# Kernel optimization log

Measured on AMD Instinct MI355X. Metric: run time of the kernel, lower is better.

The kernel has to match this reference:

```python
import jax, jax.numpy as jnp
import numpy as np
from jax import lax

# Conv3d(in_dim, in_dim, kernel=(1,3,3), padding=(0,1,1)) == per-time-slice 3x3 conv mixing channels

def _conv3d(x, w, b):
    # x: [B, C, T, W, H], w: [O, I, 1, 3, 3], b: [O]
    y = lax.conv_general_dilated(
        x, w,
        window_strides=(1, 1, 1),
        padding=[(0, 0), (1, 1), (1, 1)],
        dimension_numbers=("NCDHW", "OIDHW", "NCDHW"),
    )
    return y + b[None, :, None, None, None]


def setup_inputs() -> dict:
    key = jax.random.key(0)
    ks = jax.random.split(key, 8)
    B, C, T, W, H = 8, 64, 16, 64, 64
    fan = C * 1 * 3 * 3
    bound = 1.0 / np.sqrt(fan)  # torch Conv3d default init range
    x = jax.random.normal(ks[0], (B, C, T, W, H), dtype=jnp.float32)
    wq = jax.random.uniform(ks[1], (C, C, 1, 3, 3), jnp.float32, -bound, bound)
    wk = jax.random.uniform(ks[2], (C, C, 1, 3, 3), jnp.float32, -bound, bound)
    wv = jax.random.uniform(ks[3], (C, C, 1, 3, 3), jnp.float32, -bound, bound)
    bq = jax.random.uniform(ks[4], (C,), jnp.float32, -bound, bound)
    bk = jax.random.uniform(ks[5], (C,), jnp.float32, -bound, bound)
    bv = jax.random.uniform(ks[6], (C,), jnp.float32, -bound, bound)
    # torch init is gamma=0 (identity output); use nonzero so reference exercises the full path
    gamma = jax.random.normal(ks[7], (1,), dtype=jnp.float32) * 0.1
    return {"x": x, "wq": wq, "wk": wk, "wv": wv,
            "bq": bq, "bk": bk, "bv": bv, "gamma": gamma}


def reference(x, wq, wk, wv, bq, bk, bv, gamma):
    B, C, T, W, H = x.shape
    WH = W * H
    q = _conv3d(x, wq, bq).reshape(B, C, T, WH)
    k = _conv3d(x, wk, bk).reshape(B, C, T, WH)
    v = _conv3d(x, wv, bv).reshape(B, C, T, WH)
    # Original: (q[...,:,None] @ k[...,None,:]) @ v[...,:,None]  -> rank-1 energy, no softmax.
    # Exact reassociation: out_i = q_i * sum_j(k_j * v_j), avoiding the [WH, WH] matrix.
    s = jnp.sum(k * v, axis=-1, keepdims=True)  # [B, C, T, 1]
    out = (q * s).reshape(B, C, T, W, H)
    return gamma[0] * out + x
```

## Files before the change

kernel.cpp:

```cpp
#include <hip/hip_runtime.h>
#include <hip/hip_bf16.h>
#include <stdint.h>

typedef __attribute__((ext_vector_type(8))) short bf16x8;
typedef __attribute__((ext_vector_type(4))) float f32x4v;
typedef __attribute__((ext_vector_type(16))) float f32x16;
typedef __attribute__((ext_vector_type(4))) unsigned int u32x4;

#define CH_STRIDE 65536

__device__ __forceinline__ uint16_t f2bf(float f) {
  uint32_t u = __builtin_bit_cast(uint32_t, f);
  u = (u + 0x7FFFu + ((u >> 16) & 1u)) >> 16;
  return (uint16_t)u;
}
__device__ __forceinline__ float bf2f(uint32_t b) {
  return __builtin_bit_cast(float, b << 16);
}
__device__ __forceinline__ uint16_t cvt_bf(float f) {
  return __builtin_bit_cast(uint16_t, __float2bfloat16(f));
}
__device__ __forceinline__ bf16x8 andm(bf16x8 v, uint32_t m) {
  u32x4 u = __builtin_bit_cast(u32x4, v);
  u[0] &= m; u[1] &= m; u[2] &= m; u[3] &= m;
  return __builtin_bit_cast(bf16x8, u);
}

#define MFMA32(a, b, c) __builtin_amdgcn_mfma_f32_32x32x16_bf16(a, b, c, 0, 0, 0)
#define WAIT0 asm volatile("s_waitcnt vmcnt(0) lgkmcnt(0)" ::: "memory")
#define BAR __builtin_amdgcn_s_barrier()
#define SCHED0 __builtin_amdgcn_sched_barrier(0)

#define LDSX6  (6 * 8 * 66 * 16)
#define LDSK   (6 * 8 * 64 * 16)

__device__ __forceinline__ void gld16(const void* g, void* l) {
  __builtin_amdgcn_global_load_lds(
      (const __attribute__((address_space(1))) uint32_t*)g,
      (__attribute__((address_space(3))) uint32_t*)l, 16, 0, 0);
}

__device__ __forceinline__ bf16x8 ldx(const uint8_t* ldsx, int row, int oct, int ci) {
  return *(const bf16x8*)(ldsx + (uint32_t)((row * 8 + oct) * 66 + ci) * 16u);
}
__device__ __forceinline__ bf16x8 ldx64(const uint8_t* ldsx, int row, int oct, int ci) {
  return *(const bf16x8*)(ldsx + (uint32_t)((row * 8 + oct) * 64 + ci) * 16u);
}
__device__ __forceinline__ bf16x8 ldw_kv(const uint8_t* ldsw, int oct, int rowloc) {
  return *(const bf16x8*)(ldsw + (uint32_t)(oct * 128 + rowloc) * 16u);
}
__device__ __forceinline__ bf16x8 ldw_q(const uint8_t* ldsw, int oct, int row) {
  return *(const bf16x8*)(ldsw + (uint32_t)(oct * 64 + row) * 16u);
}

__device__ __forceinline__ void stage_unit66(uint8_t* ldsx, const float* xs, int w0, int u) {
  int row = u >> 7, oct = (u >> 4) & 7, g = u & 15;
  int w = w0 - 1 + row;
  uint32_t base = (uint32_t)((row * 8 + oct) * 66 + 4 * g + 1) * 16u;
  if ((unsigned)w < 64u) {
    const float* p = xs + (size_t)(oct * 8) * CH_STRIDE + w * 64 + 4 * g;
    f32x4v v[8];
    #pragma unroll
    for (int j = 0; j < 8; ++j) v[j] = *(const f32x4v*)(p + (size_t)j * CH_STRIDE);
    #pragma unroll
    for (int c = 0; c < 4; ++c) {
      bf16x8 frag;
      #pragma unroll
      for (int q = 0; q < 4; ++q) {
        frag[2 * q]     = (short)cvt_bf(v[2 * q][c]);
        frag[2 * q + 1] = (short)cvt_bf(v[2 * q + 1][c]);
      }
      *(bf16x8*)(ldsx + base + (uint32_t)c * 16u) = frag;
    }
  } else {
    bf16x8 z = {};
    #pragma unroll
    for (int c = 0; c < 4; ++c) *(bf16x8*)(ldsx + base + (uint32_t)c * 16u) = z;
  }
}
__device__ __forceinline__ void stage_unit64(uint8_t* ldsx, const float* xs, int w0, int u) {
  int row = u >> 7, oct = (u >> 4) & 7, g = u & 15;
  int w = w0 - 1 + row;
  uint32_t base = (uint32_t)((row * 8 + oct) * 64 + 4 * g) * 16u;
  if ((unsigned)w < 64u) {
    const float* p = xs + (size_t)(oct * 8) * CH_STRIDE + w * 64 + 4 * g;
    f32x4v v[8];
    #pragma unroll
    for (int j = 0; j < 8; ++j) v[j] = *(const f32x4v*)(p + (size_t)j * CH_STRIDE);
    #pragma unroll
    for (int c = 0; c < 4; ++c) {
      bf16x8 frag;
      #pragma unroll
      for (int q = 0; q < 4; ++q) {
        frag[2 * q]     = (short)cvt_bf(v[2 * q][c]);
        frag[2 * q + 1] = (short)cvt_bf(v[2 * q + 1][c]);
      }
      *(bf16x8*)(ldsx + base + (uint32_t)c * 16u) = frag;
    }
  } else {
    bf16x8 z = {};
    #pragma unroll
    for (int c = 0; c < 4; ++c) *(bf16x8*)(ldsx + base + (uint32_t)c * 16u) = z;
  }
}
__device__ __forceinline__ void stage_halo66(uint8_t* ldsx, int tid, int nrow) {
  if (tid < nrow * 16) {
    int row = tid >> 4, rem = tid & 15;
    int oct = rem >> 1, side = rem & 1;
    bf16x8 z = {};
    *(bf16x8*)(ldsx + (uint32_t)((row * 8 + oct) * 66 + side * 65) * 16u) = z;
  }
}

__global__ void prep_weights(const float* __restrict__ wq, const float* __restrict__ wk,
                             const float* __restrict__ wv, uint16_t* __restrict__ wout) {
  int i = blockIdx.x * 256 + threadIdx.x;
  if (i >= 110592) return;
  if (i < 36864) {
    int tap = i >> 12, oct = (i >> 9) & 7, row = (i >> 3) & 63, j = i & 7;
    wout[i] = f2bf(wq[(row * 64 + oct * 8 + j) * 9 + tap]);
  } else {
    int m = i - 36864;
    int tap = m >> 13, oct = (m >> 10) & 7, rl = (m >> 3) & 127, j = m & 7;
    const float* src = (rl < 64) ? wk : wv;
    wout[i] = f2bf(src[((rl & 63) * 64 + oct * 8 + j) * 9 + tap]);
  }
}

__global__ __launch_bounds__(256, 2) void kv_s_kernel(
    const float* __restrict__ x, const uint16_t* __restrict__ wkv,
    const float* __restrict__ bk, const float* __restrict__ bv,
    float* __restrict__ s_out) {
  extern __shared__ uint8_t lds[];
  uint8_t* ldsx = lds;
  uint8_t* ldswA = lds + LDSK;
  uint8_t* ldswB = lds + LDSK + 16384;
  const int tid = threadIdx.x;
  const int l = tid & 63;
  const int ng = tid >> 6;
  int bid = (int)(blockIdx.x & 7) * 256 + (int)(blockIdx.x >> 3);
  const int rg = bid & 15, slice = bid >> 4;
  const int b = slice >> 4, t = slice & 15;
  const int w0 = rg * 4;
  const float* xs = x + ((size_t)b * 1024 + t) * 4096;
  const int lm = l & 31, lh = l >> 5;
  const uint32_t mz0 = (lm == 0) ? 0u : ~0u;
  const uint32_t mz1 = (lm == 31) ? 0u : ~0u;

  #pragma unroll
  for (int k = 0; k < 4; ++k)
    gld16(wkv + (size_t)(tid + k * 256) * 8, ldswA + (uint32_t)(tid + k * 256) * 16u);
  #pragma unroll
  for (int k = 0; k < 3; ++k) stage_unit64(ldsx, xs, w0, tid + k * 256);
  SCHED0; WAIT0; BAR; SCHED0;

  f32x16 accK[2][2], accV[2][2];
  #pragma unroll
  for (int mt = 0; mt < 2; ++mt)
    #pragma unroll
    for (int nt = 0; nt < 2; ++nt)
      #pragma unroll
      for (int q = 0; q < 16; ++q) { accK[mt][nt][q] = 0.f; accV[mt][nt][q] = 0.f; }

  #pragma unroll
  for (int tap = 0; tap < 9; ++tap) {
    const int dy = tap / 3, dx = tap % 3;
    const uint8_t* bufc = (tap & 1) ? ldswB : ldswA;
    uint8_t* bufn = (tap & 1) ? ldswA : ldswB;
    if (tap < 8) {
      #pragma unroll
      for (int k = 0; k < 4; ++k)
        gld16(wkv + ((size_t)(tap + 1) * 1024 + tid + k * 256) * 8,
              bufn + (uint32_t)(tid + k * 256) * 16u);
    }
    __builtin_amdgcn_s_setprio(1);
    #pragma unroll
    for (int s = 0; s < 4; ++s) {
      int oct = s * 2 + lh;
      bf16x8 aK0 = ldw_kv(bufc, oct, lm);
      bf16x8 aK1 = ldw_kv(bufc, oct, 32 + lm);
      bf16x8 aV0 = ldw_kv(bufc, oct, 64 + lm);
      bf16x8 aV1 = ldw_kv(bufc, oct, 96 + lm);
      bf16x8 b0  = ldx64(ldsx, ng + dy, oct, (lm + dx - 1) & 63);
      bf16x8 b1  = ldx64(ldsx, ng + dy, oct, (32 + lm + dx - 1) & 63);
      if (dx == 0) b0 = andm(b0, mz0);
      if (dx == 2) b1 = andm(b1, mz1);
      accK[0][0] = MFMA32(aK0, b0, accK[0][0]);
      accK[0][1] = MFMA32(aK0, b1, accK[0][1]);
      accK[1][0] = MFMA32(aK1, b0, accK[1][0]);
      accK[1][1] = MFMA32(aK1, b1, accK[1][1]);
      accV[0][0] = MFMA32(aV0, b0, accV[0][0]);
      accV[0][1] = MFMA32(aV0, b1, accV[0][1]);
      accV[1][0] = MFMA32(aV1, b0, accV[1][0]);
      accV[1][1] = MFMA32(aV1, b1, accV[1][1]);
    }
    __builtin_amdgcn_s_setprio(0);
    SCHED0; WAIT0; BAR; SCHED0;
  }

  __syncthreads();
  float* red = (float*)lds;
  #pragma unroll
  for (int q = 0; q < 16; ++q) {
    int cl = (q & 3) + 8 * (q >> 2) + 4 * lh;
    #pragma unroll
    for (int mt = 0; mt < 2; ++mt) {
      int c = mt * 32 + cl;
      float bkc = bk[c], bvc = bv[c];
      float p = (accK[mt][0][q] + bkc) * (accV[mt][0][q] + bvc)
              + (accK[mt][1][q] + bkc) * (accV[mt][1][q] + bvc);
      red[c * 133 + ng * 32 + lm] = p;
    }
  }
  __syncthreads();
  if (tid < 64) {
    const float* rp = red + tid * 133;
    f32x4v a4 = {0.f, 0.f, 0.f, 0.f};
    #pragma unroll
    for (int j = 0; j < 32; ++j) a4 += *(const f32x4v*)(rp + j * 4);
    atomicAdd(s_out + (b * 16 + t) * 64 + tid, a4[0] + a4[1] + a4[2] + a4[3]);
  }
}

__global__ __launch_bounds__(256, 2) void q_out_kernel(
    const float* __restrict__ x, const uint16_t* __restrict__ wq,
    const float* __restrict__ bq, const float* __restrict__ s_in,
    const float* __restrict__ gamma, float* __restrict__ out) {
  extern __shared__ uint8_t lds[];
  uint8_t* ldsx = lds;
  uint8_t* ldswA = lds + LDSX6;
  uint8_t* ldswB = lds + LDSX6 + 8192;
  const int tid = threadIdx.x;
  const int l = tid & 63, ng = tid >> 6;
  int bid = (int)(blockIdx.x & 7) * 256 + (int)(blockIdx.x >> 3);
  const int rg = bid & 15, slice = bid >> 4;
  const int b = slice >> 4, t = slice & 15;
  const int w0 = rg * 4;
  const float* xs = x + ((size_t)b * 1024 + t) * 4096;
  const int lm = l & 31, lh = l >> 5;

  #pragma unroll
  for (int k = 0; k < 2; ++k)
    gld16(wq + (size_t)(tid + k * 256) * 8, ldswA + (uint32_t)(tid + k * 256) * 16u);
  stage_halo66(ldsx, tid, 6);
  #pragma unroll
  for (int k = 0; k < 3; ++k) stage_unit66(ldsx, xs, w0, tid + k * 256);
  SCHED0; WAIT0; BAR; SCHED0;

  f32x16 acc[2][2];
  #pragma unroll
  for (int mt = 0; mt < 2; ++mt)
    #pragma unroll
    for (int nt = 0; nt < 2; ++nt)
      #pragma unroll
      for (int q = 0; q < 16; ++q) acc[mt][nt][q] = 0.f;

  #pragma unroll
  for (int tap = 0; tap < 9; ++tap) {
    const int dy = tap / 3, dx = tap % 3;
    const uint8_t* bufc = (tap & 1) ? ldswB : ldswA;
    uint8_t* bufn = (tap & 1) ? ldswA : ldswB;
    if (tap < 8) {
      #pragma unroll
      for (int k = 0; k < 2; ++k)
        gld16(wq + ((size_t)(tap + 1) * 512 + tid + k * 256) * 8,
              bufn + (uint32_t)(tid + k * 256) * 16u);
    }
    __builtin_amdgcn_s_setprio(1);
    #pragma unroll
    for (int s = 0; s < 4; ++s) {
      int oct = s * 2 + lh;
      bf16x8 a0 = ldw_q(bufc, oct, lm);
      bf16x8 a1 = ldw_q(bufc, oct, 32 + lm);
      bf16x8 b0 = ldx(ldsx, ng + dy, oct, lm + dx);
      bf16x8 b1 = ldx(ldsx, ng + dy, oct, 32 + lm + dx);
      acc[0][0] = MFMA32(a0, b0, acc[0][0]);
      acc[0][1] = MFMA32(a0, b1, acc[0][1]);
      acc[1][0] = MFMA32(a1, b0, acc[1][0]);
      acc[1][1] = MFMA32(a1, b1, acc[1][1]);
    }
    __builtin_amdgcn_s_setprio(0);
    SCHED0; WAIT0; BAR; SCHED0;
  }

  float g = gamma[0];
  const float* sb = s_in + (b * 16 + t) * 64;
  int w = w0 + ng;
  #pragma unroll
  for (int mt = 0; mt < 2; ++mt) {
    #pragma unroll
    for (int q = 0; q < 16; ++q) {
      int cl = (q & 3) + 8 * (q >> 2) + 4 * lh;
      int c  = mt * 32 + cl;
      float qb = bq[c], sc = sb[c];
      #pragma unroll
      for (int nt = 0; nt < 2; ++nt) {
        int h = nt * 32 + lm;
        uint32_t xb = (uint32_t)(((ng + 1) * 8 + (c >> 3)) * 66 + (h + 1)) * 16u
                    + (uint32_t)(c & 7) * 2u;
        float xv = bf2f(*(const uint16_t*)(ldsx + xb));
        size_t idx = ((size_t)(b * 64 + c) * 16 + t) * 4096 + (size_t)w * 64 + h;
        out[idx] = g * (acc[mt][nt][q] + qb) * sc + xv;
      }
    }
  }
}

extern "C" void kernel_launch(void* const* d_in, const int* in_sizes, int n_in,
                              void* d_out, int out_size, void* d_ws, size_t ws_size,
                              hipStream_t stream) {
  const float* x   = (const float*)d_in[0];
  const float* wq  = (const float*)d_in[1];
  const float* wk  = (const float*)d_in[2];
  const float* wv  = (const float*)d_in[3];
  const float* bq  = (const float*)d_in[4];
  const float* bk  = (const float*)d_in[5];
  const float* bv  = (const float*)d_in[6];
  const float* gam = (const float*)d_in[7];

  uint16_t* wbf = (uint16_t*)d_ws;
  float* sbuf   = (float*)((uint8_t*)d_ws + 221184);

  hipMemsetAsync(sbuf, 0, 8 * 16 * 64 * sizeof(float), stream);
  prep_weights<<<(110592 + 255) / 256, 256, 0, stream>>>(wq, wk, wv, wbf);
  kv_s_kernel<<<2048, 256, LDSK + 32768, stream>>>(x, wbf + 36864, bk, bv, sbuf);
  q_out_kernel<<<2048, 256, LDSX6 + 16384, stream>>>(x, wbf, bq, sbuf, gam, (float*)d_out);
}
```

Baseline: 149.8 us.

## Read K/V weights directly from global memory instead of double-buffered LDS

The kv_s_kernel no longer stages the per-tap K/V weight slices into double-buffered LDS with per-tap barriers. Each lane now loads its weight fragments straight from global memory, relying on L1/L2 caching. This removes 32 KB of LDS and nine barriers per block, and launch bounds are raised from 2 to 3 blocks per CU to raise occupancy. In exchange, weight loads now carry global-memory latency inside the MFMA loop, and register pressure may rise under the tighter launch bound.

```diff
diff --git a/kernel.cpp b/kernel.cpp
--- a/kernel.cpp
+++ b/kernel.cpp
@@ -46,11 +46,11 @@
 __device__ __forceinline__ bf16x8 ldx64(const uint8_t* ldsx, int row, int oct, int ci) {
   return *(const bf16x8*)(ldsx + (uint32_t)((row * 8 + oct) * 64 + ci) * 16u);
 }
-__device__ __forceinline__ bf16x8 ldw_kv(const uint8_t* ldsw, int oct, int rowloc) {
-  return *(const bf16x8*)(ldsw + (uint32_t)(oct * 128 + rowloc) * 16u);
-}
 __device__ __forceinline__ bf16x8 ldw_q(const uint8_t* ldsw, int oct, int row) {
   return *(const bf16x8*)(ldsw + (uint32_t)(oct * 64 + row) * 16u);
+}
+__device__ __forceinline__ bf16x8 ldw_g(const uint16_t* wkv, int tap, int oct, int rowloc) {
+  return *(const bf16x8*)(wkv + ((size_t)(tap * 8 + oct) * 128 + rowloc) * 8);
 }
 
 __device__ __forceinline__ void stage_unit66(uint8_t* ldsx, const float* xs, int w0, int u) {
@@ -127,14 +127,12 @@
   }
 }
 
-__global__ __launch_bounds__(256, 2) void kv_s_kernel(
+__global__ __launch_bounds__(256, 3) void kv_s_kernel(
     const float* __restrict__ x, const uint16_t* __restrict__ wkv,
     const float* __restrict__ bk, const float* __restrict__ bv,
     float* __restrict__ s_out) {
   extern __shared__ uint8_t lds[];
   uint8_t* ldsx = lds;
-  uint8_t* ldswA = lds + LDSK;
-  uint8_t* ldswB = lds + LDSK + 16384;
   const int tid = threadIdx.x;
   const int l = tid & 63;
   const int ng = tid >> 6;
@@ -148,11 +146,8 @@
   const uint32_t mz1 = (lm == 31) ? 0u : ~0u;
 
   #pragma unroll
-  for (int k = 0; k < 4; ++k)
-    gld16(wkv + (size_t)(tid + k * 256) * 8, ldswA + (uint32_t)(tid + k * 256) * 16u);
-  #pragma unroll
   for (int k = 0; k < 3; ++k) stage_unit64(ldsx, xs, w0, tid + k * 256);
-  SCHED0; WAIT0; BAR; SCHED0;
+  __syncthreads();
 
   f32x16 accK[2][2], accV[2][2];
   #pragma unroll
@@ -165,22 +160,13 @@
   #pragma unroll
   for (int tap = 0; tap < 9; ++tap) {
     const int dy = tap / 3, dx = tap % 3;
-    const uint8_t* bufc = (tap & 1) ? ldswB : ldswA;
-    uint8_t* bufn = (tap & 1) ? ldswA : ldswB;
-    if (tap < 8) {
-      #pragma unroll
-      for (int k = 0; k < 4; ++k)
-        gld16(wkv + ((size_t)(tap + 1) * 1024 + tid + k * 256) * 8,
-              bufn + (uint32_t)(tid + k * 256) * 16u);
-    }
-    __builtin_amdgcn_s_setprio(1);
     #pragma unroll
     for (int s = 0; s < 4; ++s) {
       int oct = s * 2 + lh;
-      bf16x8 aK0 = ldw_kv(bufc, oct, lm);
-      bf16x8 aK1 = ldw_kv(bufc, oct, 32 + lm);
-      bf16x8 aV0 = ldw_kv(bufc, oct, 64 + lm);
-      bf16x8 aV1 = ldw_kv(bufc, oct, 96 + lm);
+      bf16x8 aK0 = ldw_g(wkv, tap, oct, lm);
+      bf16x8 aK1 = ldw_g(wkv, tap, oct, 32 + lm);
+      bf16x8 aV0 = ldw_g(wkv, tap, oct, 64 + lm);
+      bf16x8 aV1 = ldw_g(wkv, tap, oct, 96 + lm);
       bf16x8 b0  = ldx64(ldsx, ng + dy, oct, (lm + dx - 1) & 63);
       bf16x8 b1  = ldx64(ldsx, ng + dy, oct, (32 + lm + dx - 1) & 63);
       if (dx == 0) b0 = andm(b0, mz0);
@@ -194,8 +180,6 @@
       accV[1][0] = MFMA32(aV1, b0, accV[1][0]);
       accV[1][1] = MFMA32(aV1, b1, accV[1][1]);
     }
-    __builtin_amdgcn_s_setprio(0);
-    SCHED0; WAIT0; BAR; SCHED0;
   }
 
   __syncthreads();
@@ -323,6 +307,6 @@
 
   hipMemsetAsync(sbuf, 0, 8 * 16 * 64 * sizeof(float), stream);
   prep_weights<<<(110592 + 255) / 256, 256, 0, stream>>>(wq, wk, wv, wbf);
-  kv_s_kernel<<<2048, 256, LDSK + 32768, stream>>>(x, wbf + 36864, bk, bv, sbuf);
+  kv_s_kernel<<<2048, 256, LDSK, stream>>>(x, wbf + 36864, bk, bv, sbuf);
   q_out_kernel<<<2048, 256, LDSX6 + 16384, stream>>>(x, wbf, bq, sbuf, gam, (float*)d_out);
 }
```

New measurement: 219.9 us. 1.47x slower.
